# Optimization experiments

Measured on AMD Instinct MI355X. Metric: run time of the kernel, lower is better.

The kernel has to match this reference:

```python
import jax, jax.numpy as jnp
import numpy as np

N_NODES = 50000
N_EDGES = 800000
F_IN = 128
HIDDEN = 32
HEADS = 4
F_OUT = 64
NEG_SLOPE = 0.2


def setup_inputs() -> dict:
    key = jax.random.key(0)
    ks = jax.random.split(key, 9)
    x = jax.random.normal(ks[0], (N_NODES, F_IN), dtype=jnp.float32)
    edge_index = jax.random.randint(ks[1], (2, N_EDGES), 0, N_NODES, dtype=jnp.int64)
    edge_weight = jax.random.uniform(ks[2], (N_EDGES,), dtype=jnp.float32)
    # GATConv parameters
    W = jax.random.normal(ks[3], (F_IN, HEADS * HIDDEN), dtype=jnp.float32) * (1.0 / np.sqrt(F_IN))
    a_src = jax.random.normal(ks[4], (HEADS, HIDDEN), dtype=jnp.float32) * 0.1
    a_dst = jax.random.normal(ks[5], (HEADS, HIDDEN), dtype=jnp.float32) * 0.1
    bias = jnp.zeros((HEADS * HIDDEN,), dtype=jnp.float32)
    # output linear
    W2 = jax.random.normal(ks[6], (HEADS * HIDDEN, F_OUT), dtype=jnp.float32) * (1.0 / np.sqrt(HEADS * HIDDEN))
    b2 = jnp.zeros((F_OUT,), dtype=jnp.float32)
    return {"x": x, "edge_index": edge_index, "edge_weight": edge_weight,
            "W": W, "a_src": a_src, "a_dst": a_dst, "bias": bias,
            "W2": W2, "b2": b2}


def reference(x, edge_index, edge_weight, W, a_src, a_dst, bias, W2, b2):
    src, dst = edge_index[0], edge_index[1]
    # linear transform per head: [N, H, C]
    h = (x @ W).reshape(-1, HEADS, HIDDEN)
    # per-node attention logits: [N, H]
    alpha_s = jnp.einsum('nhc,hc->nh', h, a_src)
    alpha_d = jnp.einsum('nhc,hc->nh', h, a_dst)
    # per-edge scores: [E, H]
    e = alpha_s[src] + alpha_d[dst]
    e = jnp.where(e >= 0, e, NEG_SLOPE * e)  # LeakyReLU(0.2)
    # segment softmax over destination neighborhoods
    m = jax.ops.segment_max(e, dst, num_segments=N_NODES)  # [N, H]
    ex = jnp.exp(e - m[dst])
    denom = jax.ops.segment_sum(ex, dst, num_segments=N_NODES)  # [N, H]
    alpha = ex / (denom[dst] + 1e-16)  # [E, H]
    # weighted scatter-add aggregation: [N, H, C]
    msgs = alpha[:, :, None] * h[src]
    out = jax.ops.segment_sum(msgs, dst, num_segments=N_NODES)
    out = out.reshape(-1, HEADS * HIDDEN) + bias
    out = jax.nn.elu(out)
    return out @ W2 + b2
```

## Files before the change

kernel.cpp:

```cpp
#include <hip/hip_runtime.h>

#define N_NODES 50000
#define N_EDGES 800000
#define F_IN 128
#define HH 128
#define HEADS 4
#define HIDDEN 32
#define F_OUT 64
#define NEG_SLOPE 0.2f
#define CAP 64

#define NODE_BLOCKS ((N_NODES + 31) / 32)
#define FILL_BLOCKS ((N_EDGES / 4 + 255) / 256)

__device__ __forceinline__ unsigned short f2bf(float f) {
    unsigned int u = __float_as_uint(f);
    u = (u + 0x7FFFu + ((u >> 16) & 1u)) >> 16;
    return (unsigned short)u;
}

__global__ __launch_bounds__(256) void k_node_fill(
    const float* __restrict__ x, const float* __restrict__ W,
    const float* __restrict__ a_src, const float* __restrict__ a_dst,
    unsigned short* __restrict__ h_bf,
    float* __restrict__ as_out, float* __restrict__ ad_out,
    const int* __restrict__ ei, int* __restrict__ cursor, int* __restrict__ bucket)
{
    __shared__ float xs[32][F_IN];

    if (blockIdx.x >= NODE_BLOCKS) {
        int e0 = ((blockIdx.x - NODE_BLOCKS) * 256 + threadIdx.x) * 4;
        if (e0 < N_EDGES) {
            int4 s4 = *(const int4*)&ei[e0];
            int4 d4 = *(const int4*)&ei[N_EDGES + e0];
            bucket[(size_t)d4.x * CAP + (atomicAdd(&cursor[d4.x], 1) & (CAP - 1))] = s4.x;
            bucket[(size_t)d4.y * CAP + (atomicAdd(&cursor[d4.y], 1) & (CAP - 1))] = s4.y;
            bucket[(size_t)d4.z * CAP + (atomicAdd(&cursor[d4.z], 1) & (CAP - 1))] = s4.z;
            bucket[(size_t)d4.w * CAP + (atomicAdd(&cursor[d4.w], 1) & (CAP - 1))] = s4.w;
        }
        return;
    }

    const int tid  = threadIdx.x;
    const int base = blockIdx.x * 32;

    for (int i = tid; i < 32 * 32; i += 256) {
        int r = i >> 5, c4 = i & 31;
        int n = base + r;
        float4 v = (n < N_NODES) ? *(const float4*)&x[(size_t)n * F_IN + c4 * 4]
                                 : make_float4(0.f, 0.f, 0.f, 0.f);
        *(float4*)&xs[r][c4 * 4] = v;
    }
    __syncthreads();

    const int cg = tid & 31;
    const int q  = tid >> 5;

    float4 acc[4] = {};
    for (int k4 = 0; k4 < 32; ++k4) {
        const float* wr = &W[(k4 * 4) * HH + cg * 4];
        float4 w0 = *(const float4*)(wr);
        float4 w1 = *(const float4*)(wr + HH);
        float4 w2 = *(const float4*)(wr + 2 * HH);
        float4 w3 = *(const float4*)(wr + 3 * HH);
        #pragma unroll
        for (int j = 0; j < 4; ++j) {
            float4 xv = *(const float4*)&xs[q * 4 + j][k4 * 4];
            acc[j].x = fmaf(xv.x, w0.x, acc[j].x); acc[j].y = fmaf(xv.x, w0.y, acc[j].y);
            acc[j].z = fmaf(xv.x, w0.z, acc[j].z); acc[j].w = fmaf(xv.x, w0.w, acc[j].w);
            acc[j].x = fmaf(xv.y, w1.x, acc[j].x); acc[j].y = fmaf(xv.y, w1.y, acc[j].y);
            acc[j].z = fmaf(xv.y, w1.z, acc[j].z); acc[j].w = fmaf(xv.y, w1.w, acc[j].w);
            acc[j].x = fmaf(xv.z, w2.x, acc[j].x); acc[j].y = fmaf(xv.z, w2.y, acc[j].y);
            acc[j].z = fmaf(xv.z, w2.z, acc[j].z); acc[j].w = fmaf(xv.z, w2.w, acc[j].w);
            acc[j].x = fmaf(xv.w, w3.x, acc[j].x); acc[j].y = fmaf(xv.w, w3.y, acc[j].y);
            acc[j].z = fmaf(xv.w, w3.z, acc[j].z); acc[j].w = fmaf(xv.w, w3.w, acc[j].w);
        }
    }

    const float4 as4 = *(const float4*)&a_src[cg * 4];
    const float4 ad4 = *(const float4*)&a_dst[cg * 4];
    const int hd = cg >> 3;

    #pragma unroll
    for (int j = 0; j < 4; ++j) {
        int n = base + q * 4 + j;
        if (n >= N_NODES) continue;

        ushort4 hv;
        hv.x = f2bf(acc[j].x); hv.y = f2bf(acc[j].y);
        hv.z = f2bf(acc[j].z); hv.w = f2bf(acc[j].w);
        *(ushort4*)&h_bf[(size_t)n * HH + cg * 4] = hv;

        float ps = acc[j].x * as4.x + acc[j].y * as4.y + acc[j].z * as4.z + acc[j].w * as4.w;
        float pd = acc[j].x * ad4.x + acc[j].y * ad4.y + acc[j].z * ad4.z + acc[j].w * ad4.w;
        #pragma unroll
        for (int off = 1; off < 8; off <<= 1) {
            ps += __shfl_xor(ps, off, 64);
            pd += __shfl_xor(pd, off, 64);
        }
        if ((cg & 7) == 0) {
            as_out[n * HEADS + hd] = ps;
            ad_out[n * HEADS + hd] = pd;
        }
    }
}

__global__ __launch_bounds__(256) void k_gather(
    const int* __restrict__ cnt_arr, const int* __restrict__ bucket,
    const float* __restrict__ as_, const float* __restrict__ ad_,
    const unsigned short* __restrict__ h_bf, float* __restrict__ agg)
{
    int gid = blockIdx.x * 256 + threadIdx.x;
    int n = gid >> 6;
    if (n >= N_NODES) return;
    const int lane = gid & 63;
    const int hd  = lane >> 4;
    const int e16 = lane & 15;

    const float advv = ad_[n * 4 + hd];
    const int cnt = cnt_arr[n];
    const int* brow = &bucket[(size_t)n * CAP];

    float accx = 0.f, accy = 0.f, sum = 0.f;

    for (int cb = 0; cb < cnt; cb += 16) {
        int m = cnt - cb; if (m > 16) m = 16;
        int s = 0; float exown = 0.f;
        if (e16 < m) {
            s = brow[cb + e16];
            float lg = as_[s * 4 + hd] + advv;
            lg = lg >= 0.f ? lg : NEG_SLOPE * lg;
            exown = __expf(lg);
        }

#define GAT_BODY(j)                                                            \
        {                                                                      \
            float al = __shfl(exown, (hd << 4) + (j));                         \
            int   sj = __shfl(s,     (hd << 4) + (j));                         \
            unsigned int hv = *(const unsigned int*)&h_bf[(size_t)sj * HH + lane * 2]; \
            sum += al;                                                         \
            accx = fmaf(al, __uint_as_float((hv & 0xFFFFu) << 16), accx);      \
            accy = fmaf(al, __uint_as_float(hv & 0xFFFF0000u), accy);          \
        }

        if (m == 16) {
            #pragma unroll
            for (int j = 0; j < 16; ++j) GAT_BODY(j)
        } else {
            for (int j = 0; j < m; ++j) GAT_BODY(j)
        }
#undef GAT_BODY
    }

    float inv = 1.f / (sum + 1e-16f);
    *(float2*)&agg[(size_t)n * HH + lane * 2] = make_float2(accx * inv, accy * inv);
}

__global__ __launch_bounds__(256) void k_output(
    const float* __restrict__ agg, const float* __restrict__ bias,
    const float* __restrict__ W2, const float* __restrict__ b2,
    float* __restrict__ out)
{
    __shared__ float eb[64][132];

    const int tid  = threadIdx.x;
    const int base = blockIdx.x * 64;

    for (int i = tid; i < 64 * 32; i += 256) {
        int r = i >> 5, c4 = i & 31;
        int n = base + r;
        float4 v = (n < N_NODES) ? *(const float4*)&agg[(size_t)n * HH + c4 * 4]
                                 : make_float4(0.f, 0.f, 0.f, 0.f);
        float4 b = *(const float4*)&bias[c4 * 4];
        v.x += b.x; v.y += b.y; v.z += b.z; v.w += b.w;
        v.x = v.x > 0.f ? v.x : __expf(v.x) - 1.f;
        v.y = v.y > 0.f ? v.y : __expf(v.y) - 1.f;
        v.z = v.z > 0.f ? v.z : __expf(v.z) - 1.f;
        v.w = v.w > 0.f ? v.w : __expf(v.w) - 1.f;
        *(float4*)&eb[r][c4 * 4] = v;
    }
    __syncthreads();

    const int cg = tid & 15;
    const int q  = tid >> 4;

    float4 b2v = *(const float4*)&b2[cg * 4];
    float4 acc[4] = { b2v, b2v, b2v, b2v };
    for (int k4 = 0; k4 < 32; ++k4) {
        const float* wr = &W2[(k4 * 4) * F_OUT + cg * 4];
        float4 w0 = *(const float4*)(wr);
        float4 w1 = *(const float4*)(wr + F_OUT);
        float4 w2 = *(const float4*)(wr + 2 * F_OUT);
        float4 w3 = *(const float4*)(wr + 3 * F_OUT);
        #pragma unroll
        for (int j = 0; j < 4; ++j) {
            float4 xv = *(const float4*)&eb[q * 4 + j][k4 * 4];
            acc[j].x = fmaf(xv.x, w0.x, acc[j].x); acc[j].y = fmaf(xv.x, w0.y, acc[j].y);
            acc[j].z = fmaf(xv.x, w0.z, acc[j].z); acc[j].w = fmaf(xv.x, w0.w, acc[j].w);
            acc[j].x = fmaf(xv.y, w1.x, acc[j].x); acc[j].y = fmaf(xv.y, w1.y, acc[j].y);
            acc[j].z = fmaf(xv.y, w1.z, acc[j].z); acc[j].w = fmaf(xv.y, w1.w, acc[j].w);
            acc[j].x = fmaf(xv.z, w2.x, acc[j].x); acc[j].y = fmaf(xv.z, w2.y, acc[j].y);
            acc[j].z = fmaf(xv.z, w2.z, acc[j].z); acc[j].w = fmaf(xv.z, w2.w, acc[j].w);
            acc[j].x = fmaf(xv.w, w3.x, acc[j].x); acc[j].y = fmaf(xv.w, w3.y, acc[j].y);
            acc[j].z = fmaf(xv.w, w3.z, acc[j].z); acc[j].w = fmaf(xv.w, w3.w, acc[j].w);
        }
    }
    #pragma unroll
    for (int j = 0; j < 4; ++j) {
        int n = base + q * 4 + j;
        if (n < N_NODES)
            *(float4*)&out[(size_t)n * F_OUT + cg * 4] = acc[j];
    }
}

extern "C" void kernel_launch(void* const* d_in, const int* in_sizes, int n_in,
                              void* d_out, int out_size, void* d_ws, size_t ws_size,
                              hipStream_t stream)
{
    const float* x     = (const float*)d_in[0];
    const int*   ei    = (const int*)  d_in[1];
    const float* W     = (const float*)d_in[3];
    const float* a_src = (const float*)d_in[4];
    const float* a_dst = (const float*)d_in[5];
    const float* bias  = (const float*)d_in[6];
    const float* W2    = (const float*)d_in[7];
    const float* b2    = (const float*)d_in[8];
    float* out = (float*)d_out;

    char* ws = (char*)d_ws;
    unsigned short* h_bf = (unsigned short*)ws;
    float* as_   = (float*)(ws + (size_t)N_NODES * HH * 2);
    float* ad_   = as_ + (size_t)N_NODES * HEADS;
    int*   cursor= (int*)(ad_ + (size_t)N_NODES * HEADS);
    int*   bucket= cursor + N_NODES;
    float* agg   = (float*)(bucket + (size_t)N_NODES * CAP);

    hipMemsetAsync(cursor, 0, (size_t)N_NODES * sizeof(int), stream);

    k_node_fill<<<NODE_BLOCKS + FILL_BLOCKS, 256, 0, stream>>>(
        x, W, a_src, a_dst, h_bf, as_, ad_, ei, cursor, bucket);
    k_gather<<<(N_NODES * 64 + 255) / 256, 256, 0, stream>>>(cursor, bucket, as_, ad_, h_bf, agg);
    k_output<<<(N_NODES + 63) / 64, 256, 0, stream>>>(agg, bias, W2, b2, out);
}
```

Before: 134.8 us.

## Compute node projection x@W with bf16 MFMA instead of scalar FMAs

Replaces the FP32 FMA loop for x@W in the fused node/fill kernel with bf16 MFMA 16x16x32 instructions. x is converted to bf16 into padded shared memory, and W fragments are loaded and converted to bf16 per wave. Attention logits are reduced from the MFMA accumulator layout with 16-lane shuffles. This lowers ALU cost for the projection but adds bf16 rounding of the inputs, and each block now does strided scalar loads of W.

```diff
diff --git a/kernel.cpp b/kernel.cpp
--- a/kernel.cpp
+++ b/kernel.cpp
@@ -13,6 +13,9 @@
 #define NODE_BLOCKS ((N_NODES + 31) / 32)
 #define FILL_BLOCKS ((N_EDGES / 4 + 255) / 256)
 
+typedef __attribute__((ext_vector_type(8))) short short8v;
+typedef __attribute__((ext_vector_type(4))) float float4v;
+
 __device__ __forceinline__ unsigned short f2bf(float f) {
     unsigned int u = __float_as_uint(f);
     u = (u + 0x7FFFu + ((u >> 16) & 1u)) >> 16;
@@ -26,7 +29,7 @@
     float* __restrict__ as_out, float* __restrict__ ad_out,
     const int* __restrict__ ei, int* __restrict__ cursor, int* __restrict__ bucket)
 {
-    __shared__ float xs[32][F_IN];
+    __shared__ __align__(16) unsigned short xs[32][136];
 
     if (blockIdx.x >= NODE_BLOCKS) {
         int e0 = ((blockIdx.x - NODE_BLOCKS) * 256 + threadIdx.x) * 4;
@@ -49,58 +52,68 @@
         int n = base + r;
         float4 v = (n < N_NODES) ? *(const float4*)&x[(size_t)n * F_IN + c4 * 4]
                                  : make_float4(0.f, 0.f, 0.f, 0.f);
-        *(float4*)&xs[r][c4 * 4] = v;
+        ushort4 hv;
+        hv.x = f2bf(v.x); hv.y = f2bf(v.y); hv.z = f2bf(v.z); hv.w = f2bf(v.w);
+        *(ushort4*)&xs[r][c4 * 4] = hv;
     }
     __syncthreads();
 
-    const int cg = tid & 31;
-    const int q  = tid >> 5;
-
-    float4 acc[4] = {};
-    for (int k4 = 0; k4 < 32; ++k4) {
-        const float* wr = &W[(k4 * 4) * HH + cg * 4];
-        float4 w0 = *(const float4*)(wr);
-        float4 w1 = *(const float4*)(wr + HH);
-        float4 w2 = *(const float4*)(wr + 2 * HH);
-        float4 w3 = *(const float4*)(wr + 3 * HH);
+    const int w    = tid >> 6;
+    const int lane = tid & 63;
+    const int l15  = lane & 15;
+    const int l4   = lane >> 4;
+
+    short8v bfrag[4][2];
+    #pragma unroll
+    for (int ks = 0; ks < 4; ++ks) {
         #pragma unroll
-        for (int j = 0; j < 4; ++j) {
-            float4 xv = *(const float4*)&xs[q * 4 + j][k4 * 4];
-            acc[j].x = fmaf(xv.x, w0.x, acc[j].x); acc[j].y = fmaf(xv.x, w0.y, acc[j].y);
-            acc[j].z = fmaf(xv.x, w0.z, acc[j].z); acc[j].w = fmaf(xv.x, w0.w, acc[j].w);
-            acc[j].x = fmaf(xv.y, w1.x, acc[j].x); acc[j].y = fmaf(xv.y, w1.y, acc[j].y);
-            acc[j].z = fmaf(xv.y, w1.z, acc[j].z); acc[j].w = fmaf(xv.y, w1.w, acc[j].w);
-            acc[j].x = fmaf(xv.z, w2.x, acc[j].x); acc[j].y = fmaf(xv.z, w2.y, acc[j].y);
-            acc[j].z = fmaf(xv.z, w2.z, acc[j].z); acc[j].w = fmaf(xv.z, w2.w, acc[j].w);
-            acc[j].x = fmaf(xv.w, w3.x, acc[j].x); acc[j].y = fmaf(xv.w, w3.y, acc[j].y);
-            acc[j].z = fmaf(xv.w, w3.z, acc[j].z); acc[j].w = fmaf(xv.w, w3.w, acc[j].w);
-        }
-    }
-
-    const float4 as4 = *(const float4*)&a_src[cg * 4];
-    const float4 ad4 = *(const float4*)&a_dst[cg * 4];
-    const int hd = cg >> 3;
-
-    #pragma unroll
-    for (int j = 0; j < 4; ++j) {
-        int n = base + q * 4 + j;
-        if (n >= N_NODES) continue;
-
-        ushort4 hv;
-        hv.x = f2bf(acc[j].x); hv.y = f2bf(acc[j].y);
-        hv.z = f2bf(acc[j].z); hv.w = f2bf(acc[j].w);
-        *(ushort4*)&h_bf[(size_t)n * HH + cg * 4] = hv;
-
-        float ps = acc[j].x * as4.x + acc[j].y * as4.y + acc[j].z * as4.z + acc[j].w * as4.w;
-        float pd = acc[j].x * ad4.x + acc[j].y * ad4.y + acc[j].z * ad4.z + acc[j].w * ad4.w;
+        for (int nn = 0; nn < 2; ++nn) {
+            int c  = w * 32 + nn * 16 + l15;
+            int kb = ks * 32 + l4 * 8;
+            short8v b;
+            #pragma unroll
+            for (int j = 0; j < 8; ++j)
+                b[j] = (short)f2bf(W[(kb + j) * HH + c]);
+            bfrag[ks][nn] = b;
+        }
+    }
+
+    float4v acc[2][2] = {};
+    #pragma unroll
+    for (int ks = 0; ks < 4; ++ks) {
+        short8v a0 = *(const short8v*)&xs[l15][ks * 32 + l4 * 8];
+        short8v a1 = *(const short8v*)&xs[16 + l15][ks * 32 + l4 * 8];
+        acc[0][0] = __builtin_amdgcn_mfma_f32_16x16x32_bf16(a0, bfrag[ks][0], acc[0][0], 0, 0, 0);
+        acc[0][1] = __builtin_amdgcn_mfma_f32_16x16x32_bf16(a0, bfrag[ks][1], acc[0][1], 0, 0, 0);
+        acc[1][0] = __builtin_amdgcn_mfma_f32_16x16x32_bf16(a1, bfrag[ks][0], acc[1][0], 0, 0, 0);
+        acc[1][1] = __builtin_amdgcn_mfma_f32_16x16x32_bf16(a1, bfrag[ks][1], acc[1][1], 0, 0, 0);
+    }
+
+    const float as0 = a_src[w * 32 + l15],      ad0 = a_dst[w * 32 + l15];
+    const float as1 = a_src[w * 32 + 16 + l15], ad1 = a_dst[w * 32 + 16 + l15];
+
+    #pragma unroll
+    for (int m = 0; m < 2; ++m) {
         #pragma unroll
-        for (int off = 1; off < 8; off <<= 1) {
-            ps += __shfl_xor(ps, off, 64);
-            pd += __shfl_xor(pd, off, 64);
-        }
-        if ((cg & 7) == 0) {
-            as_out[n * HEADS + hd] = ps;
-            ad_out[n * HEADS + hd] = pd;
+        for (int reg = 0; reg < 4; ++reg) {
+            int node = base + m * 16 + l4 * 4 + reg;
+            float v0 = acc[m][0][reg];
+            float v1 = acc[m][1][reg];
+            if (node < N_NODES) {
+                h_bf[(size_t)node * HH + w * 32 + l15]      = f2bf(v0);
+                h_bf[(size_t)node * HH + w * 32 + 16 + l15] = f2bf(v1);
+            }
+            float ps = v0 * as0 + v1 * as1;
+            float pd = v0 * ad0 + v1 * ad1;
+            #pragma unroll
+            for (int off = 1; off < 16; off <<= 1) {
+                ps += __shfl_xor(ps, off, 16);
+                pd += __shfl_xor(pd, off, 16);
+            }
+            if (l15 == 0 && node < N_NODES) {
+                as_out[node * HEADS + w] = ps;
+                ad_out[node * HEADS + w] = pd;
+            }
         }
     }
 }
```

Result: no change. 133.2 us (-1.2%).
